# Kernel optimization log

Hardware: AMD Instinct MI355X
Metric: run time of the kernel (lower is better)

The kernel has to match this reference:

```python
import jax, jax.numpy as jnp
import numpy as np

N = 100000   # nodes
E = 1600000  # edges
IN = 32      # in_channels
ED = 16      # edge_dim
G = 128      # num graphs in batch
NEG = 0.01   # LeakyReLU default slope

def lrelu(v):
    return jnp.where(v > 0, v, NEG * v)

def gine_conv(x, src, dst, edge_attr, We, be, Wa, ba, Wb, bb):
    # PyG GINEConv (eps=0): out = nn(x + sum_{j->i} relu(x_j + lin(edge_attr)))
    e = edge_attr @ We + be                      # [E, d]
    m = jax.nn.relu(x[src] + e)                  # gather + add + relu
    agg = jax.ops.segment_sum(m, dst, num_segments=x.shape[0])
    h = x + agg
    return lrelu(h @ Wa + ba) @ Wb + bb

def setup_inputs() -> dict:
    key = jax.random.key(0)
    ks = jax.random.split(key, 24)
    w = lambda k, shape: (jax.random.normal(k, shape, dtype=jnp.float32) * 0.05)
    inp = {
        "x": jax.random.normal(ks[0], (N, IN), dtype=jnp.float32),
        "edge_index": jax.random.randint(ks[1], (2, E), 0, N),
        "edge_attr": jax.random.normal(ks[2], (E, ED), dtype=jnp.float32),
        "batch": jnp.sort(jax.random.randint(ks[3], (N,), 0, G)),
        # conv1: edge lin ED->IN, nn IN->32->64
        "We1": w(ks[4], (ED, IN)), "be1": w(ks[5], (IN,)),
        "W1a": w(ks[6], (IN, 32)), "b1a": w(ks[7], (32,)),
        "W1b": w(ks[8], (32, 64)), "b1b": w(ks[9], (64,)),
        # conv2: edge lin ED->64, nn 64->128->256
        "We2": w(ks[10], (ED, 64)), "be2": w(ks[11], (64,)),
        "W2a": w(ks[12], (64, 128)), "b2a": w(ks[13], (128,)),
        "W2b": w(ks[14], (128, 256)), "b2b": w(ks[15], (256,)),
        # head
        "Wf0": w(ks[16], (256, 128)), "bf0": w(ks[17], (128,)),
        "Wf1": w(ks[18], (128, 64)), "bf1": w(ks[19], (64,)),
        "Wf2": w(ks[20], (64, 32)), "bf2": w(ks[21], (32,)),
        "Wr": w(ks[22], (32, 1)), "br": w(ks[23], (1,)),
    }
    return inp

def reference(x, edge_index, edge_attr, batch,
              We1, be1, W1a, b1a, W1b, b1b,
              We2, be2, W2a, b2a, W2b, b2b,
              Wf0, bf0, Wf1, bf1, Wf2, bf2, Wr, br):
    src, dst = edge_index[0], edge_index[1]
    h = gine_conv(x, src, dst, edge_attr, We1, be1, W1a, b1a, W1b, b1b)
    h = lrelu(h)
    h = gine_conv(h, src, dst, edge_attr, We2, be2, W2a, b2a, W2b, b2b)
    h = lrelu(h)
    # global_add_pool over graph ids
    g = jax.ops.segment_sum(h, batch, num_segments=G)   # [G, 256]
    g = lrelu(g @ Wf0 + bf0)
    # dropout: identity (inference reference)
    g = lrelu(g @ Wf1 + bf1)
    g = lrelu(g @ Wf2 + bf2)
    out = (g @ Wr + br)[:, 0]                           # squeeze(dim=1)
    return out
```

## Files before the change

kernel.cpp:

```cpp
#include <hip/hip_runtime.h>

__device__ __forceinline__ float lrelu(float v){ return v > 0.f ? v : 0.01f*v; }

typedef __attribute__((ext_vector_type(8))) short v8s;
typedef __attribute__((ext_vector_type(4))) float v4f;

__device__ __forceinline__ unsigned short f2bf(float f){
    union{float f; unsigned int i;} v; v.f = f;
    unsigned int u = v.i;
    return (unsigned short)((u + 0x7fffu + ((u >> 16) & 1u)) >> 16);
}
__device__ __forceinline__ unsigned int pack2(float a, float b){
    return (unsigned int)f2bf(a) | ((unsigned int)f2bf(b) << 16);
}
__device__ __forceinline__ float bflo(unsigned int u){
    union{unsigned int i; float f;} v; v.i = u << 16; return v.f;
}
__device__ __forceinline__ float bfhi(unsigned int u){
    union{unsigned int i; float f;} v; v.i = u & 0xffff0000u; return v.f;
}
__device__ __forceinline__ float bf2f(unsigned short s){
    union{unsigned int i; float f;} v; v.i = ((unsigned int)s) << 16; return v.f;
}

__global__ __launch_bounds__(256) void k_hist(
    const int* __restrict__ ei, int* __restrict__ deg, int E)
{
    int e = blockIdx.x * 256 + threadIdx.x;
    if (e >= E) return;
    atomicAdd(&deg[ei[E + e]], 1);
}

__global__ __launch_bounds__(256) void k_scan1(
    const int* __restrict__ deg, int* __restrict__ rowptr,
    int* __restrict__ bsum, int N)
{
    __shared__ int sh[256];
    int t = threadIdx.x;
    int i = blockIdx.x * 256 + t;
    int v = (i < N) ? deg[i] : 0;
    sh[t] = v;
    __syncthreads();
    #pragma unroll
    for (int off = 1; off < 256; off <<= 1) {
        int add = (t >= off) ? sh[t - off] : 0;
        __syncthreads();
        sh[t] += add;
        __syncthreads();
    }
    if (i < N) rowptr[i] = sh[t] - v;
    if (t == 255) bsum[blockIdx.x] = sh[t];
}

__global__ __launch_bounds__(512) void k_scan2(int* __restrict__ bsum, int nb)
{
    __shared__ int sh[512];
    int t = threadIdx.x;
    int v = (t < nb) ? bsum[t] : 0;
    sh[t] = v;
    __syncthreads();
    #pragma unroll
    for (int off = 1; off < 512; off <<= 1) {
        int add = (t >= off) ? sh[t - off] : 0;
        __syncthreads();
        sh[t] += add;
        __syncthreads();
    }
    if (t < nb) bsum[t] = sh[t] - v;
}

__global__ __launch_bounds__(256) void k_scan3(
    int* __restrict__ rowptr, int* __restrict__ cursor,
    const int* __restrict__ bsum, int N)
{
    int i = blockIdx.x * 256 + threadIdx.x;
    if (i >= N) return;
    int rp = rowptr[i] + bsum[i >> 8];
    rowptr[i] = rp;
    cursor[i] = rp;
}

__global__ __launch_bounds__(256) void k_castx(
    const float* __restrict__ x, unsigned int* __restrict__ xb, int M8)
{
    int i = blockIdx.x * 256 + threadIdx.x;
    if (i >= M8) return;
    const float4* p = reinterpret_cast<const float4*>(x) + (size_t)i * 2;
    float4 a = p[0], b = p[1];
    uint4 o;
    o.x = pack2(a.x, a.y); o.y = pack2(a.z, a.w);
    o.z = pack2(b.x, b.y); o.w = pack2(b.z, b.w);
    reinterpret_cast<uint4*>(xb)[i] = o;
}

__global__ __launch_bounds__(256) void k_castw(
    const float* __restrict__ W2a, const float* __restrict__ W2b,
    const float* __restrict__ We1, const float* __restrict__ We2,
    unsigned short* __restrict__ W2aT, unsigned short* __restrict__ W2bT,
    unsigned short* __restrict__ WeT1, unsigned short* __restrict__ WeT2)
{
    int i = blockIdx.x * 256 + threadIdx.x;
    if (i < 128 * 64) {
        int n = i >> 6, k = i & 63;
        W2aT[i] = f2bf(W2a[k * 128 + n]);
    }
    int j = i - 128 * 64;
    if (j >= 0 && j < 256 * 128) {
        int n = j >> 7, k = j & 127;
        W2bT[j] = f2bf(W2b[k * 256 + n]);
    }
    int q1 = i - (128 * 64 + 256 * 128);
    if (q1 >= 0 && q1 < 32 * 32) {
        int cch = q1 >> 5, k = q1 & 31;
        WeT1[q1] = (k < 16) ? f2bf(We1[k * 32 + cch]) : (unsigned short)0;
    }
    int q2 = q1 - 32 * 32;
    if (q2 >= 0 && q2 < 64 * 32) {
        int cch = q2 >> 5, k = q2 & 31;
        WeT2[q2] = (k < 16) ? f2bf(We2[k * 64 + cch]) : (unsigned short)0;
    }
}

__global__ __launch_bounds__(256) void k_scatter(
    const int* __restrict__ ei, const float* __restrict__ ea,
    int* __restrict__ cursor, int2* __restrict__ csr2,
    uint4* __restrict__ eab, int E)
{
    int e = blockIdx.x * 256 + threadIdx.x;
    if (e >= E) return;
    int s = ei[e];
    int d = ei[E + e];
    int slot = atomicAdd(&cursor[d], 1);
    const float4* p = reinterpret_cast<const float4*>(ea) + (size_t)e * 4;
    float4 a = p[0], b = p[1], c = p[2], f = p[3];
    uint4 o0, o1;
    o0.x = pack2(a.x, a.y); o0.y = pack2(a.z, a.w);
    o0.z = pack2(b.x, b.y); o0.w = pack2(b.z, b.w);
    o1.x = pack2(c.x, c.y); o1.y = pack2(c.z, c.w);
    o1.z = pack2(f.x, f.y); o1.w = pack2(f.z, f.w);
    eab[(size_t)slot * 2]     = o0;
    eab[(size_t)slot * 2 + 1] = o1;
    int2 r; r.x = s; r.y = d;
    csr2[slot] = r;
}

#define AGG_SPW 64

__global__ __launch_bounds__(256) void k_agg2(
    const unsigned short* __restrict__ xb,
    const uint4* __restrict__ eab,
    const unsigned short* __restrict__ WeT,
    const float* __restrict__ be,
    const int2* __restrict__ csr2, float* __restrict__ agg, int E)
{
    __shared__ __align__(16) float lds[4][2][16][68];
    const int tid  = threadIdx.x;
    const int wv   = tid >> 6;
    const int lane = tid & 63;
    const int lid  = lane & 15;
    const int quad = lane >> 4;
    const int wave = __builtin_amdgcn_readfirstlane((blockIdx.x * 256 + tid) >> 6);
    const int s0 = wave * AGG_SPW;
    if (s0 >= E) return;
    const int nsl = (s0 + AGG_SPW <= E) ? AGG_SPW : E - s0;

    v8s af0 = *reinterpret_cast<const v8s*>(WeT + lid * 32 + quad * 8);
    v8s af1 = *reinterpret_cast<const v8s*>(WeT + (16 + lid) * 32 + quad * 8);
    v8s af2 = *reinterpret_cast<const v8s*>(WeT + (32 + lid) * 32 + quad * 8);
    v8s af3 = *reinterpret_cast<const v8s*>(WeT + (48 + lid) * 32 + quad * 8);
    const float biasc = be[lane];
    const int2*  cp = csr2 + s0;
    const uint4* ep = eab + (size_t)s0 * 2;

    unsigned short xv[2][16];
    int dsv[2][16];
    float acc = 0.f;
    int   cur = cp[0].y;
    bool  owned = false;

    auto GATHER = [&](int t) {
        const int base = t * 16;
        const int cnt = nsl - base;
        #pragma unroll
        for (int e = 0; e < 16; ++e) {
            int ee = (e < cnt) ? e : cnt - 1;
            int2 r = cp[base + ee];
            dsv[t & 1][e] = r.y;
            xv[t & 1][e] = xb[(unsigned)r.x * 64u + (unsigned)lane];
        }
    };
    auto MFMA = [&](int t) {
        int sl = t * 16 + lid;
        if (sl > nsl - 1) sl = nsl - 1;
        uint4 bw = {0u, 0u, 0u, 0u};
        if (quad < 2) bw = ep[2 * sl + quad];
        union { uint4 u; v8s s; } uu; uu.u = bw;
        v8s bf = uu.s;
        v4f d0 = {0.f, 0.f, 0.f, 0.f}, d1 = d0, d2 = d0, d3 = d0;
        d0 = __builtin_amdgcn_mfma_f32_16x16x32_bf16(af0, bf, d0, 0, 0, 0);
        d1 = __builtin_amdgcn_mfma_f32_16x16x32_bf16(af1, bf, d1, 0, 0, 0);
        d2 = __builtin_amdgcn_mfma_f32_16x16x32_bf16(af2, bf, d2, 0, 0, 0);
        d3 = __builtin_amdgcn_mfma_f32_16x16x32_bf16(af3, bf, d3, 0, 0, 0);
        float* lp = &lds[wv][t & 1][lid][quad * 4];
        *reinterpret_cast<v4f*>(lp)      = d0;
        *reinterpret_cast<v4f*>(lp + 16) = d1;
        *reinterpret_cast<v4f*>(lp + 32) = d2;
        *reinterpret_cast<v4f*>(lp + 48) = d3;
    };
    auto ACCUM = [&](int t) {
        const int cnt = nsl - t * 16;
        #pragma unroll
        for (int e = 0; e < 16; ++e) {
            if (e < cnt) {
                float ls = lds[wv][t & 1][e][lane];
                float m = ls + biasc + bf2f(xv[t & 1][e]);
                m = m > 0.f ? m : 0.f;
                int d = dsv[t & 1][e];
                if (d != cur) {
                    if (owned) agg[(unsigned)cur * 64u + lane] = acc;
                    else       atomicAdd(&agg[(unsigned)cur * 64u + lane], acc);
                    acc = 0.f; cur = d; owned = true;
                }
                acc += m;
            }
        }
    };

    GATHER(0); MFMA(0);
    #pragma unroll
    for (int t = 0; t < 4; ++t) {
        if (t * 16 < nsl) {
            if ((t + 1) < 4 && (t + 1) * 16 < nsl) { GATHER(t + 1); MFMA(t + 1); }
            ACCUM(t);
        }
    }
    atomicAdd(&agg[(unsigned)cur * 64u + lane], acc);
}

__global__ __launch_bounds__(256) void k_agg1(
    const unsigned short* __restrict__ xb,
    const uint4* __restrict__ eab,
    const unsigned short* __restrict__ WeT,
    const float* __restrict__ be,
    const int2* __restrict__ csr2, float* __restrict__ agg, int E)
{
    __shared__ __align__(16) float lds[4][2][16][36];
    const int tid  = threadIdx.x;
    const int wv   = tid >> 6;
    const int lane = tid & 63;
    const int lid  = lane & 15;
    const int quad = lane >> 4;
    const int c    = lane & 31;
    const int sub  = lane >> 5;
    const int wave = __builtin_amdgcn_readfirstlane((blockIdx.x * 256 + tid) >> 6);
    const int s0 = wave * AGG_SPW;
    if (s0 >= E) return;
    const int nsl = (s0 + AGG_SPW <= E) ? AGG_SPW : E - s0;

    v8s af0 = *reinterpret_cast<const v8s*>(WeT + lid * 32 + quad * 8);
    v8s af1 = *reinterpret_cast<const v8s*>(WeT + (16 + lid) * 32 + quad * 8);
    const float biasc = be[c];
    const int2*  cp = csr2 + s0;
    const uint4* ep = eab + (size_t)s0 * 2;

    unsigned short xv[2][8];
    int dsv[2][8];
    float acc = 0.f;
    int cur = cp[(sub < nsl) ? sub : 0].y;

    auto GATHER = [&](int t) {
        #pragma unroll
        for (int i = 0; i < 8; ++i) {
            int e = t * 16 + 2 * i + sub;
            int ee = (e < nsl) ? e : nsl - 1;
            int2 r = cp[ee];
            dsv[t & 1][i] = r.y;
            xv[t & 1][i] = xb[(unsigned)r.x * 32u + (unsigned)c];
        }
    };
    auto MFMA = [&](int t) {
        int sl = t * 16 + lid;
        if (sl > nsl - 1) sl = nsl - 1;
        uint4 bw = {0u, 0u, 0u, 0u};
        if (quad < 2) bw = ep[2 * sl + quad];
        union { uint4 u; v8s s; } uu; uu.u = bw;
        v8s bf = uu.s;
        v4f d0 = {0.f, 0.f, 0.f, 0.f}, d1 = d0;
        d0 = __builtin_amdgcn_mfma_f32_16x16x32_bf16(af0, bf, d0, 0, 0, 0);
        d1 = __builtin_amdgcn_mfma_f32_16x16x32_bf16(af1, bf, d1, 0, 0, 0);
        float* lp = &lds[wv][t & 1][lid][quad * 4];
        *reinterpret_cast<v4f*>(lp)      = d0;
        *reinterpret_cast<v4f*>(lp + 16) = d1;
    };
    auto ACCUM = [&](int t) {
        #pragma unroll
        for (int i = 0; i < 8; ++i) {
            int e = t * 16 + 2 * i + sub;
            if (e < nsl) {
                float ls = lds[wv][t & 1][2 * i + sub][c];
                float m = ls + biasc + bf2f(xv[t & 1][i]);
                m = m > 0.f ? m : 0.f;
                int d = dsv[t & 1][i];
                if (d != cur) {
                    atomicAdd(&agg[(unsigned)cur * 32u + c], acc);
                    acc = 0.f; cur = d;
                }
                acc += m;
            }
        }
    };

    GATHER(0); MFMA(0);
    #pragma unroll
    for (int t = 0; t < 4; ++t) {
        if (t * 16 < nsl) {
            if ((t + 1) < 4 && (t + 1) * 16 < nsl) { GATHER(t + 1); MFMA(t + 1); }
            ACCUM(t);
        }
    }
    atomicAdd(&agg[(unsigned)cur * 32u + c], acc);
}

__global__ __launch_bounds__(256, 4) void k_mlp1(
    const float* __restrict__ x, const float* __restrict__ agg1,
    const float* __restrict__ W1a, const float* __restrict__ b1a,
    const float* __restrict__ W1b, const float* __restrict__ b1b,
    float* __restrict__ h1, unsigned int* __restrict__ h1b, int N)
{
    __shared__ float ts[64][33];
    const int tid = threadIdx.x;
    const int n0 = blockIdx.x * 64;
    const int row = tid & 63;
    const int grp = __builtin_amdgcn_readfirstlane(tid >> 6);
    const int g = n0 + row;

    float hv[32];
    if (g < N) {
        const float4* xp = reinterpret_cast<const float4*>(x) + (size_t)g * 8;
        const float4* ap = reinterpret_cast<const float4*>(agg1) + (size_t)g * 8;
        #pragma unroll
        for (int q = 0; q < 8; ++q) {
            float4 a = xp[q], b = ap[q];
            hv[4*q+0]=a.x+b.x; hv[4*q+1]=a.y+b.y;
            hv[4*q+2]=a.z+b.z; hv[4*q+3]=a.w+b.w;
        }
    } else {
        #pragma unroll
        for (int q = 0; q < 32; ++q) hv[q] = 0.f;
    }

    {
        const int c0 = grp * 8;
        float acc[8];
        #pragma unroll
        for (int i = 0; i < 8; ++i) acc[i] = b1a[c0 + i];
        for (int k = 0; k < 32; ++k) {
            float h = hv[k];
            const float* w = W1a + k*32 + c0;
            #pragma unroll
            for (int i = 0; i < 8; ++i) acc[i] = fmaf(h, w[i], acc[i]);
        }
        #pragma unroll
        for (int i = 0; i < 8; ++i) ts[row][c0 + i] = lrelu(acc[i]);
    }
    __syncthreads();

    {
        const int c0 = grp * 16;
        float acc[16];
        #pragma unroll
        for (int i = 0; i < 16; ++i) acc[i] = b1b[c0 + i];
        for (int k = 0; k < 32; ++k) {
            float tv = ts[row][k];
            const float* w = W1b + k*64 + c0;
            #pragma unroll
            for (int i = 0; i < 16; ++i) acc[i] = fmaf(tv, w[i], acc[i]);
        }
        if (g < N) {
            #pragma unroll
            for (int i = 0; i < 16; ++i) acc[i] = lrelu(acc[i]);
            float4* op = reinterpret_cast<float4*>(h1) + (size_t)g*16 + (c0>>2);
            #pragma unroll
            for (int q = 0; q < 4; ++q) {
                float4 o;
                o.x = acc[4*q+0]; o.y = acc[4*q+1];
                o.z = acc[4*q+2]; o.w = acc[4*q+3];
                op[q] = o;
            }
            uint4 p0, p1;
            p0.x = pack2(acc[0],  acc[1]);  p0.y = pack2(acc[2],  acc[3]);
            p0.z = pack2(acc[4],  acc[5]);  p0.w = pack2(acc[6],  acc[7]);
            p1.x = pack2(acc[8],  acc[9]);  p1.y = pack2(acc[10], acc[11]);
            p1.z = pack2(acc[12], acc[13]); p1.w = pack2(acc[14], acc[15]);
            uint4* bp = reinterpret_cast<uint4*>(h1b + (size_t)g*32 + (c0>>1));
            bp[0] = p0; bp[1] = p1;
        }
    }
}

__global__ __launch_bounds__(256) void k_mlp2(
    const float* __restrict__ h1, const float* __restrict__ agg2,
    const unsigned short* __restrict__ W2aT, const float* __restrict__ b2a,
    const unsigned short* __restrict__ W2bT, const float* __restrict__ b2b,
    unsigned short* __restrict__ h2b, int N)
{
    __shared__ unsigned short hs[64][72];
    __shared__ unsigned short ts[64][136];
    const int tid = threadIdx.x;
    const int n0 = blockIdx.x * 64;

    {
        int r = tid >> 2, cseg = (tid & 3) * 16;
        int g = n0 + r;
        uint4 o0 = {0,0,0,0}, o1 = {0,0,0,0};
        if (g < N) {
            const float4* xp = reinterpret_cast<const float4*>(h1)
                               + (size_t)g*16 + (cseg>>2);
            const float4* ap = reinterpret_cast<const float4*>(agg2)
                               + (size_t)g*16 + (cseg>>2);
            float4 a0=xp[0], a1=xp[1], a2=xp[2], a3=xp[3];
            float4 b0=ap[0], b1=ap[1], b2=ap[2], b3=ap[3];
            o0.x = pack2(a0.x+b0.x, a0.y+b0.y); o0.y = pack2(a0.z+b0.z, a0.w+b0.w);
            o0.z = pack2(a1.x+b1.x, a1.y+b1.y); o0.w = pack2(a1.z+b1.z, a1.w+b1.w);
            o1.x = pack2(a2.x+b2.x, a2.y+b2.y); o1.y = pack2(a2.z+b2.z, a2.w+b2.w);
            o1.z = pack2(a3.x+b3.x, a3.y+b3.y); o1.w = pack2(a3.z+b3.z, a3.w+b3.w);
        }
        uint4* dp = reinterpret_cast<uint4*>(&hs[r][cseg]);
        dp[0] = o0; dp[1] = o1;
    }
    __syncthreads();

    const int wv   = __builtin_amdgcn_readfirstlane(tid >> 6);
    const int lane = tid & 63;
    const int lid  = lane & 15;
    const int quad = lane >> 4;

    v8s afA0 = *reinterpret_cast<const v8s*>(&hs[wv*16 + lid][quad*8]);
    v8s afA1 = *reinterpret_cast<const v8s*>(&hs[wv*16 + lid][32 + quad*8]);
    #pragma unroll
    for (int nt = 0; nt < 8; ++nt) {
        v4f acc = {0.f, 0.f, 0.f, 0.f};
        const unsigned short* wp = W2aT + (nt*16 + lid)*64 + quad*8;
        v8s b0 = *reinterpret_cast<const v8s*>(wp);
        v8s b1 = *reinterpret_cast<const v8s*>(wp + 32);
        acc = __builtin_amdgcn_mfma_f32_16x16x32_bf16(afA0, b0, acc, 0, 0, 0);
        acc = __builtin_amdgcn_mfma_f32_16x16x32_bf16(afA1, b1, acc, 0, 0, 0);
        float bias = b2a[nt*16 + lid];
        #pragma unroll
        for (int i = 0; i < 4; ++i) {
            float v = lrelu(acc[i] + bias);
            ts[wv*16 + quad*4 + i][nt*16 + lid] = f2bf(v);
        }
    }
    __syncthreads();

    v8s afB[4];
    #pragma unroll
    for (int ks = 0; ks < 4; ++ks)
        afB[ks] = *reinterpret_cast<const v8s*>(&ts[wv*16 + lid][ks*32 + quad*8]);
    const int gbase = n0 + wv*16 + quad*4;
    #pragma unroll 4
    for (int nt = 0; nt < 16; ++nt) {
        v4f acc = {0.f, 0.f, 0.f, 0.f};
        const unsigned short* wp = W2bT + (nt*16 + lid)*128 + quad*8;
        #pragma unroll
        for (int ks = 0; ks < 4; ++ks) {
            v8s bf = *reinterpret_cast<const v8s*>(wp + ks*32);
            acc = __builtin_amdgcn_mfma_f32_16x16x32_bf16(afB[ks], bf, acc, 0, 0, 0);
        }
        float bias = b2b[nt*16 + lid];
        #pragma unroll
        for (int i = 0; i < 4; ++i) {
            int g = gbase + i;
            if (g < N) {
                float v = lrelu(acc[i] + bias);
                h2b[(size_t)g*256 + nt*16 + lid] = f2bf(v);
            }
        }
    }
}

__global__ __launch_bounds__(256) void k_pool(
    const unsigned int* __restrict__ h2b, const int* __restrict__ batch,
    float* __restrict__ g, int N)
{
    int tid = threadIdx.x;
    int c2 = tid & 127;
    int h = tid >> 7;
    int base = blockIdx.x * 128;
    int n0 = base + h;
    int nend = base + 128; if (nend > N) nend = N;
    if (n0 >= N) return;
    float acc0 = 0.f, acc1 = 0.f;
    int cur = batch[n0];
    for (int n = n0; n < nend; n += 2) {
        int b = batch[n];
        unsigned int hv = h2b[(size_t)n * 128 + c2];
        if (b != cur) {
            atomicAdd(&g[(unsigned)cur * 256 + 2*c2],     acc0);
            atomicAdd(&g[(unsigned)cur * 256 + 2*c2 + 1], acc1);
            acc0 = acc1 = 0.f; cur = b;
        }
        acc0 += bflo(hv); acc1 += bfhi(hv);
    }
    atomicAdd(&g[(unsigned)cur * 256 + 2*c2],     acc0);
    atomicAdd(&g[(unsigned)cur * 256 + 2*c2 + 1], acc1);
}

__global__ __launch_bounds__(256) void k_head(
    const float* __restrict__ g,
    const float* __restrict__ Wf0, const float* __restrict__ bf0,
    const float* __restrict__ Wf1, const float* __restrict__ bf1,
    const float* __restrict__ Wf2, const float* __restrict__ bf2,
    const float* __restrict__ Wr,  const float* __restrict__ br,
    float* __restrict__ out)
{
    __shared__ float buf[256];
    __shared__ float t0[128];
    __shared__ float t1[64];
    __shared__ float t2[32];
    int gid = blockIdx.x, tid = threadIdx.x;
    buf[tid] = g[(size_t)gid*256 + tid];
    __syncthreads();
    if (tid < 128) {
        float acc = bf0[tid];
        for (int k = 0; k < 256; ++k) acc = fmaf(buf[k], Wf0[k*128 + tid], acc);
        t0[tid] = lrelu(acc);
    }
    __syncthreads();
    if (tid < 64) {
        float acc = bf1[tid];
        for (int k = 0; k < 128; ++k) acc = fmaf(t0[k], Wf1[k*64 + tid], acc);
        t1[tid] = lrelu(acc);
    }
    __syncthreads();
    if (tid < 32) {
        float acc = bf2[tid];
        for (int k = 0; k < 64; ++k) acc = fmaf(t1[k], Wf2[k*32 + tid], acc);
        t2[tid] = lrelu(acc);
    }
    __syncthreads();
    if (tid == 0) {
        float acc = br[0];
        for (int k = 0; k < 32; ++k) acc = fmaf(t2[k], Wr[k], acc);
        out[gid] = acc;
    }
}

extern "C" void kernel_launch(void* const* d_in, const int* in_sizes, int n_in,
                              void* d_out, int out_size, void* d_ws, size_t ws_size,
                              hipStream_t stream)
{
    const float* x     = (const float*)d_in[0];
    const int*   ei    = (const int*)d_in[1];
    const float* ea    = (const float*)d_in[2];
    const int*   batch = (const int*)d_in[3];
    const float* We1=(const float*)d_in[4],  *be1=(const float*)d_in[5];
    const float* W1a=(const float*)d_in[6],  *b1a=(const float*)d_in[7];
    const float* W1b=(const float*)d_in[8],  *b1b=(const float*)d_in[9];
    const float* We2=(const float*)d_in[10], *be2=(const float*)d_in[11];
    const float* W2a=(const float*)d_in[12], *b2a=(const float*)d_in[13];
    const float* W2b=(const float*)d_in[14], *b2b=(const float*)d_in[15];
    const float* Wf0=(const float*)d_in[16], *bf0=(const float*)d_in[17];
    const float* Wf1=(const float*)d_in[18], *bf1=(const float*)d_in[19];
    const float* Wf2=(const float*)d_in[20], *bf2=(const float*)d_in[21];
    const float* Wr =(const float*)d_in[22], *br =(const float*)d_in[23];

    const int N = in_sizes[0] / 32;
    const int E = in_sizes[1] / 2;
    const int G = out_size;
    const int nb = (N + 255) / 256;
    const int nb64 = (N + 63) / 64;

    char* p = (char*)d_ws;
    int*   deg     = (int*)p;                 p += (size_t)N * 4;
    float* gbuf    = (float*)p;               p += (size_t)G * 256 * 4;
    float* agg1    = (float*)p;               p += (size_t)N * 32 * 4;
    float* agg2    = (float*)p;               p += (size_t)N * 64 * 4;
    size_t zero_bytes = (size_t)(p - (char*)d_ws);
    int*   rowptr  = (int*)p;                 p += (size_t)N * 4;
    int*   cursor  = (int*)p;                 p += (size_t)N * 4;
    int*   bsum    = (int*)p;                 p += 512 * 4;
    p = (char*)(((uintptr_t)p + 15) & ~(uintptr_t)15);
    int2*  csr2    = (int2*)p;                p += (size_t)E * 8;
    uint4* eab     = (uint4*)p;               p += (size_t)E * 32;
    unsigned short* xb   = (unsigned short*)p; p += (size_t)N * 32 * 2;
    float* h1      = (float*)p;               p += (size_t)N * 64 * 4;
    unsigned int*   h1b  = (unsigned int*)p;  p += (size_t)N * 64 * 2;
    unsigned short* W2aT = (unsigned short*)p; p += 128 * 64 * 2;
    unsigned short* W2bT = (unsigned short*)p; p += 256 * 128 * 2;
    unsigned short* WeT1 = (unsigned short*)p; p += 32 * 32 * 2;
    unsigned short* WeT2 = (unsigned short*)p; p += 64 * 32 * 2;
    unsigned short* h2b  = (unsigned short*)p; p += (size_t)N * 256 * 2;

    hipMemsetAsync(d_ws, 0, zero_bytes, stream);

    int eb = (E + 255) / 256;

    k_hist   <<<eb, 256, 0, stream>>>(ei, deg, E);
    k_scan1  <<<nb, 256, 0, stream>>>(deg, rowptr, bsum, N);
    k_scan2  <<<1, 512, 0, stream>>>(bsum, nb);
    k_scan3  <<<nb, 256, 0, stream>>>(rowptr, cursor, bsum, N);
    {
        int M8 = N * 32 / 8;
        k_castx<<<(M8 + 255) / 256, 256, 0, stream>>>(x, (unsigned int*)xb, M8);
    }
    {
        int tot = 128*64 + 256*128 + 32*32 + 64*32;
        k_castw<<<(tot + 255) / 256, 256, 0, stream>>>(W2a, W2b, We1, We2,
                                                       W2aT, W2bT, WeT1, WeT2);
    }
    k_scatter<<<eb, 256, 0, stream>>>(ei, ea, cursor, csr2, eab, E);

    {
        int waves = (E + AGG_SPW - 1) / AGG_SPW;
        int blocks = (waves + 3) / 4;
        k_agg1<<<blocks, 256, 0, stream>>>(xb, eab, WeT1, be1, csr2, agg1, E);
    }
    k_mlp1<<<nb64, 256, 0, stream>>>(x, agg1, W1a, b1a, W1b, b1b, h1,
                                     (unsigned int*)h1b, N);

    {
        int waves = (E + AGG_SPW - 1) / AGG_SPW;
        int blocks = (waves + 3) / 4;
        k_agg2<<<blocks, 256, 0, stream>>>((const unsigned short*)h1b, eab, WeT2,
                                           be2, csr2, agg2, E);
    }
    k_mlp2<<<nb64, 256, 0, stream>>>(h1, agg2, W2aT, b2a, W2bT, b2b, h2b, N);

    k_pool<<<(N + 127) / 128, 256, 0, stream>>>((const unsigned int*)h2b, batch,
                                                gbuf, N);
    k_head<<<G, 256, 0, stream>>>(gbuf, Wf0, bf0, Wf1, bf1, Wf2, bf2, Wr, br,
                                  (float*)d_out);
}
```

Baseline: 626.3 us.

## Interleave edge index and features into 64B records; drop fp32 h1 buffer

Combines the per-slot (src,dst) pair and bf16 edge attributes into one cache-line-aligned 64-byte record so the aggregation kernels touch a single stream per edge. It also removes the fp32 copy of the first-layer output, and the second MLP reads the bf16 copy for its residual. The padding raises total edge-record bytes written and read. Reading h1 in bf16 slightly reduces the precision of the residual sum.

```diff
diff --git a/kernel.cpp b/kernel.cpp
--- a/kernel.cpp
+++ b/kernel.cpp
@@ -123,8 +123,7 @@
 
 __global__ __launch_bounds__(256) void k_scatter(
     const int* __restrict__ ei, const float* __restrict__ ea,
-    int* __restrict__ cursor, int2* __restrict__ csr2,
-    uint4* __restrict__ eab, int E)
+    int* __restrict__ cursor, uint4* __restrict__ recs, int E)
 {
     int e = blockIdx.x * 256 + threadIdx.x;
     if (e >= E) return;
@@ -133,25 +132,25 @@
     int slot = atomicAdd(&cursor[d], 1);
     const float4* p = reinterpret_cast<const float4*>(ea) + (size_t)e * 4;
     float4 a = p[0], b = p[1], c = p[2], f = p[3];
-    uint4 o0, o1;
+    uint4 o0, o1, o2, o3;
     o0.x = pack2(a.x, a.y); o0.y = pack2(a.z, a.w);
     o0.z = pack2(b.x, b.y); o0.w = pack2(b.z, b.w);
     o1.x = pack2(c.x, c.y); o1.y = pack2(c.z, c.w);
     o1.z = pack2(f.x, f.y); o1.w = pack2(f.z, f.w);
-    eab[(size_t)slot * 2]     = o0;
-    eab[(size_t)slot * 2 + 1] = o1;
-    int2 r; r.x = s; r.y = d;
-    csr2[slot] = r;
+    o2.x = (unsigned)s; o2.y = (unsigned)d; o2.z = 0u; o2.w = 0u;
+    o3.x = 0u; o3.y = 0u; o3.z = 0u; o3.w = 0u;
+    uint4* rp = recs + (size_t)slot * 4;
+    rp[0] = o0; rp[1] = o1; rp[2] = o2; rp[3] = o3;
 }
 
 #define AGG_SPW 64
 
 __global__ __launch_bounds__(256) void k_agg2(
     const unsigned short* __restrict__ xb,
-    const uint4* __restrict__ eab,
+    const uint4* __restrict__ recs,
     const unsigned short* __restrict__ WeT,
     const float* __restrict__ be,
-    const int2* __restrict__ csr2, float* __restrict__ agg, int E)
+    float* __restrict__ agg, int E)
 {
     __shared__ __align__(16) float lds[4][2][16][68];
     const int tid  = threadIdx.x;
@@ -169,13 +168,12 @@
     v8s af2 = *reinterpret_cast<const v8s*>(WeT + (32 + lid) * 32 + quad * 8);
     v8s af3 = *reinterpret_cast<const v8s*>(WeT + (48 + lid) * 32 + quad * 8);
     const float biasc = be[lane];
-    const int2*  cp = csr2 + s0;
-    const uint4* ep = eab + (size_t)s0 * 2;
+    const uint4* rp = recs + (size_t)s0 * 4;
 
     unsigned short xv[2][16];
     int dsv[2][16];
     float acc = 0.f;
-    int   cur = cp[0].y;
+    int   cur = reinterpret_cast<const int2*>(rp + 2)->y;
     bool  owned = false;
 
     auto GATHER = [&](int t) {
@@ -184,7 +182,7 @@
         #pragma unroll
         for (int e = 0; e < 16; ++e) {
             int ee = (e < cnt) ? e : cnt - 1;
-            int2 r = cp[base + ee];
+            int2 r = *reinterpret_cast<const int2*>(rp + (base + ee) * 4 + 2);
             dsv[t & 1][e] = r.y;
             xv[t & 1][e] = xb[(unsigned)r.x * 64u + (unsigned)lane];
         }
@@ -193,7 +191,7 @@
         int sl = t * 16 + lid;
         if (sl > nsl - 1) sl = nsl - 1;
         uint4 bw = {0u, 0u, 0u, 0u};
-        if (quad < 2) bw = ep[2 * sl + quad];
+        if (quad < 2) bw = rp[sl * 4 + quad];
         union { uint4 u; v8s s; } uu; uu.u = bw;
         v8s bf = uu.s;
         v4f d0 = {0.f, 0.f, 0.f, 0.f}, d1 = d0, d2 = d0, d3 = d0;
@@ -239,10 +237,10 @@
 
 __global__ __launch_bounds__(256) void k_agg1(
     const unsigned short* __restrict__ xb,
-    const uint4* __restrict__ eab,
+    const uint4* __restrict__ recs,
     const unsigned short* __restrict__ WeT,
     const float* __restrict__ be,
-    const int2* __restrict__ csr2, float* __restrict__ agg, int E)
+    float* __restrict__ agg, int E)
 {
     __shared__ __align__(16) float lds[4][2][16][36];
     const int tid  = threadIdx.x;
@@ -260,20 +258,19 @@
     v8s af0 = *reinterpret_cast<const v8s*>(WeT + lid * 32 + quad * 8);
     v8s af1 = *reinterpret_cast<const v8s*>(WeT + (16 + lid) * 32 + quad * 8);
     const float biasc = be[c];
-    const int2*  cp = csr2 + s0;
-    const uint4* ep = eab + (size_t)s0 * 2;
+    const uint4* rp = recs + (size_t)s0 * 4;
 
     unsigned short xv[2][8];
     int dsv[2][8];
     float acc = 0.f;
-    int cur = cp[(sub < nsl) ? sub : 0].y;
+    int cur = reinterpret_cast<const int2*>(rp + ((sub < nsl) ? sub : 0) * 4 + 2)->y;
 
     auto GATHER = [&](int t) {
         #pragma unroll
         for (int i = 0; i < 8; ++i) {
             int e = t * 16 + 2 * i + sub;
             int ee = (e < nsl) ? e : nsl - 1;
-            int2 r = cp[ee];
+            int2 r = *reinterpret_cast<const int2*>(rp + ee * 4 + 2);
             dsv[t & 1][i] = r.y;
             xv[t & 1][i] = xb[(unsigned)r.x * 32u + (unsigned)c];
         }
@@ -282,7 +279,7 @@
         int sl = t * 16 + lid;
         if (sl > nsl - 1) sl = nsl - 1;
         uint4 bw = {0u, 0u, 0u, 0u};
-        if (quad < 2) bw = ep[2 * sl + quad];
+        if (quad < 2) bw = rp[sl * 4 + quad];
         union { uint4 u; v8s s; } uu; uu.u = bw;
         v8s bf = uu.s;
         v4f d0 = {0.f, 0.f, 0.f, 0.f}, d1 = d0;
@@ -325,7 +322,7 @@
     const float* __restrict__ x, const float* __restrict__ agg1,
     const float* __restrict__ W1a, const float* __restrict__ b1a,
     const float* __restrict__ W1b, const float* __restrict__ b1b,
-    float* __restrict__ h1, unsigned int* __restrict__ h1b, int N)
+    unsigned int* __restrict__ h1b, int N)
 {
     __shared__ float ts[64][33];
     const int tid = threadIdx.x;
@@ -379,14 +376,6 @@
         if (g < N) {
             #pragma unroll
             for (int i = 0; i < 16; ++i) acc[i] = lrelu(acc[i]);
-            float4* op = reinterpret_cast<float4*>(h1) + (size_t)g*16 + (c0>>2);
-            #pragma unroll
-            for (int q = 0; q < 4; ++q) {
-                float4 o;
-                o.x = acc[4*q+0]; o.y = acc[4*q+1];
-                o.z = acc[4*q+2]; o.w = acc[4*q+3];
-                op[q] = o;
-            }
             uint4 p0, p1;
             p0.x = pack2(acc[0],  acc[1]);  p0.y = pack2(acc[2],  acc[3]);
             p0.z = pack2(acc[4],  acc[5]);  p0.w = pack2(acc[6],  acc[7]);
@@ -399,7 +388,7 @@
 }
 
 __global__ __launch_bounds__(256) void k_mlp2(
-    const float* __restrict__ h1, const float* __restrict__ agg2,
+    const unsigned int* __restrict__ h1b, const float* __restrict__ agg2,
     const unsigned short* __restrict__ W2aT, const float* __restrict__ b2a,
     const unsigned short* __restrict__ W2bT, const float* __restrict__ b2b,
     unsigned short* __restrict__ h2b, int N)
@@ -414,16 +403,20 @@
         int g = n0 + r;
         uint4 o0 = {0,0,0,0}, o1 = {0,0,0,0};
         if (g < N) {
-            const float4* xp = reinterpret_cast<const float4*>(h1)
-                               + (size_t)g*16 + (cseg>>2);
+            const uint4* hp = reinterpret_cast<const uint4*>(
+                                  h1b + (size_t)g*32 + (cseg>>1));
             const float4* ap = reinterpret_cast<const float4*>(agg2)
                                + (size_t)g*16 + (cseg>>2);
-            float4 a0=xp[0], a1=xp[1], a2=xp[2], a3=xp[3];
+            uint4 u0 = hp[0], u1 = hp[1];
             float4 b0=ap[0], b1=ap[1], b2=ap[2], b3=ap[3];
-            o0.x = pack2(a0.x+b0.x, a0.y+b0.y); o0.y = pack2(a0.z+b0.z, a0.w+b0.w);
-            o0.z = pack2(a1.x+b1.x, a1.y+b1.y); o0.w = pack2(a1.z+b1.z, a1.w+b1.w);
-            o1.x = pack2(a2.x+b2.x, a2.y+b2.y); o1.y = pack2(a2.z+b2.z, a2.w+b2.w);
-            o1.z = pack2(a3.x+b3.x, a3.y+b3.y); o1.w = pack2(a3.z+b3.z, a3.w+b3.w);
+            o0.x = pack2(bflo(u0.x)+b0.x, bfhi(u0.x)+b0.y);
+            o0.y = pack2(bflo(u0.y)+b0.z, bfhi(u0.y)+b0.w);
+            o0.z = pack2(bflo(u0.z)+b1.x, bfhi(u0.z)+b1.y);
+            o0.w = pack2(bflo(u0.w)+b1.z, bfhi(u0.w)+b1.w);
+            o1.x = pack2(bflo(u1.x)+b2.x, bfhi(u1.x)+b2.y);
+            o1.y = pack2(bflo(u1.y)+b2.z, bfhi(u1.y)+b2.w);
+            o1.z = pack2(bflo(u1.z)+b3.x, bfhi(u1.z)+b3.y);
+            o1.w = pack2(bflo(u1.w)+b3.z, bfhi(u1.w)+b3.w);
         }
         uint4* dp = reinterpret_cast<uint4*>(&hs[r][cseg]);
         dp[0] = o0; dp[1] = o1;
@@ -581,11 +574,9 @@
     int*   rowptr  = (int*)p;                 p += (size_t)N * 4;
     int*   cursor  = (int*)p;                 p += (size_t)N * 4;
     int*   bsum    = (int*)p;                 p += 512 * 4;
-    p = (char*)(((uintptr_t)p + 15) & ~(uintptr_t)15);
-    int2*  csr2    = (int2*)p;                p += (size_t)E * 8;
-    uint4* eab     = (uint4*)p;               p += (size_t)E * 32;
+    p = (char*)(((uintptr_t)p + 63) & ~(uintptr_t)63);
+    uint4* recs    = (uint4*)p;               p += (size_t)E * 64;
     unsigned short* xb   = (unsigned short*)p; p += (size_t)N * 32 * 2;
-    float* h1      = (float*)p;               p += (size_t)N * 64 * 4;
     unsigned int*   h1b  = (unsigned int*)p;  p += (size_t)N * 64 * 2;
     unsigned short* W2aT = (unsigned short*)p; p += 128 * 64 * 2;
     unsigned short* W2bT = (unsigned short*)p; p += 256 * 128 * 2;
@@ -610,23 +601,23 @@
         k_castw<<<(tot + 255) / 256, 256, 0, stream>>>(W2a, W2b, We1, We2,
                                                        W2aT, W2bT, WeT1, WeT2);
     }
-    k_scatter<<<eb, 256, 0, stream>>>(ei, ea, cursor, csr2, eab, E);
+    k_scatter<<<eb, 256, 0, stream>>>(ei, ea, cursor, recs, E);
 
     {
         int waves = (E + AGG_SPW - 1) / AGG_SPW;
         int blocks = (waves + 3) / 4;
-        k_agg1<<<blocks, 256, 0, stream>>>(xb, eab, WeT1, be1, csr2, agg1, E);
-    }
-    k_mlp1<<<nb64, 256, 0, stream>>>(x, agg1, W1a, b1a, W1b, b1b, h1,
+        k_agg1<<<blocks, 256, 0, stream>>>(xb, recs, WeT1, be1, agg1, E);
+    }
+    k_mlp1<<<nb64, 256, 0, stream>>>(x, agg1, W1a, b1a, W1b, b1b,
                                      (unsigned int*)h1b, N);
 
     {
         int waves = (E + AGG_SPW - 1) / AGG_SPW;
         int blocks = (waves + 3) / 4;
-        k_agg2<<<blocks, 256, 0, stream>>>((const unsigned short*)h1b, eab, WeT2,
-                                           be2, csr2, agg2, E);
-    }
-    k_mlp2<<<nb64, 256, 0, stream>>>(h1, agg2, W2aT, b2a, W2bT, b2b, h2b, N);
+        k_agg2<<<blocks, 256, 0, stream>>>((const unsigned short*)h1b, recs, WeT2,
+                                           be2, agg2, E);
+    }
+    k_mlp2<<<nb64, 256, 0, stream>>>(h1b, agg2, W2aT, b2a, W2bT, b2b, h2b, N);
 
     k_pool<<<(N + 127) / 128, 256, 0, stream>>>((const unsigned int*)h2b, batch,
                                                 gbuf, N);
```

After: 666.1 us. 6.3% more time.

## Partition edge scatter by destination range and drop fp32 h1 buffer

Applied to the files above, without the earlier changes.

The scatter kernel now has each edge chunk processed by 8 blocks. Each block keeps only the edges whose destination falls in one eighth of the node range, so the scattered writes and cursor atomics from a block land in a narrower address window and stay more cache-local. The cost is that the destination index array is read 8 times. Separately, the fp32 h1 output is removed: mlp2 now reads the bf16 h1b copy, which halves that read and removes a large write. The residual add in mlp2 therefore uses bf16-rounded h1 values, and the workspace alignment is raised to 64 bytes.

```diff
diff --git a/kernel.cpp b/kernel.cpp
--- a/kernel.cpp
+++ b/kernel.cpp
@@ -121,27 +121,37 @@
     }
 }
 
+#define RCHUNK 2048
 __global__ __launch_bounds__(256) void k_scatter(
     const int* __restrict__ ei, const float* __restrict__ ea,
     int* __restrict__ cursor, int2* __restrict__ csr2,
-    uint4* __restrict__ eab, int E)
-{
-    int e = blockIdx.x * 256 + threadIdx.x;
-    if (e >= E) return;
-    int s = ei[e];
-    int d = ei[E + e];
-    int slot = atomicAdd(&cursor[d], 1);
-    const float4* p = reinterpret_cast<const float4*>(ea) + (size_t)e * 4;
-    float4 a = p[0], b = p[1], c = p[2], f = p[3];
-    uint4 o0, o1;
-    o0.x = pack2(a.x, a.y); o0.y = pack2(a.z, a.w);
-    o0.z = pack2(b.x, b.y); o0.w = pack2(b.z, b.w);
-    o1.x = pack2(c.x, c.y); o1.y = pack2(c.z, c.w);
-    o1.z = pack2(f.x, f.y); o1.w = pack2(f.z, f.w);
-    eab[(size_t)slot * 2]     = o0;
-    eab[(size_t)slot * 2 + 1] = o1;
-    int2 r; r.x = s; r.y = d;
-    csr2[slot] = r;
+    uint4* __restrict__ eab, int E, int N)
+{
+    const int r = blockIdx.x & 7;
+    const int c = blockIdx.x >> 3;
+    const int rspan = (N + 7) >> 3;
+    const int lo = r * rspan;
+    const int hi = lo + rspan;
+    int base = c * RCHUNK;
+    int end = base + RCHUNK; if (end > E) end = E;
+    for (int e = base + threadIdx.x; e < end; e += 256) {
+        int d = ei[E + e];
+        if (d >= lo && d < hi) {
+            int s = ei[e];
+            int slot = atomicAdd(&cursor[d], 1);
+            const float4* p = reinterpret_cast<const float4*>(ea) + (size_t)e * 4;
+            float4 a = p[0], b = p[1], cc = p[2], f = p[3];
+            uint4 o0, o1;
+            o0.x = pack2(a.x, a.y);  o0.y = pack2(a.z, a.w);
+            o0.z = pack2(b.x, b.y);  o0.w = pack2(b.z, b.w);
+            o1.x = pack2(cc.x, cc.y); o1.y = pack2(cc.z, cc.w);
+            o1.z = pack2(f.x, f.y);  o1.w = pack2(f.z, f.w);
+            eab[(size_t)slot * 2]     = o0;
+            eab[(size_t)slot * 2 + 1] = o1;
+            int2 rr; rr.x = s; rr.y = d;
+            csr2[slot] = rr;
+        }
+    }
 }
 
 #define AGG_SPW 64
@@ -325,7 +335,7 @@
     const float* __restrict__ x, const float* __restrict__ agg1,
     const float* __restrict__ W1a, const float* __restrict__ b1a,
     const float* __restrict__ W1b, const float* __restrict__ b1b,
-    float* __restrict__ h1, unsigned int* __restrict__ h1b, int N)
+    unsigned int* __restrict__ h1b, int N)
 {
     __shared__ float ts[64][33];
     const int tid = threadIdx.x;
@@ -379,14 +389,6 @@
         if (g < N) {
             #pragma unroll
             for (int i = 0; i < 16; ++i) acc[i] = lrelu(acc[i]);
-            float4* op = reinterpret_cast<float4*>(h1) + (size_t)g*16 + (c0>>2);
-            #pragma unroll
-            for (int q = 0; q < 4; ++q) {
-                float4 o;
-                o.x = acc[4*q+0]; o.y = acc[4*q+1];
-                o.z = acc[4*q+2]; o.w = acc[4*q+3];
-                op[q] = o;
-            }
             uint4 p0, p1;
             p0.x = pack2(acc[0],  acc[1]);  p0.y = pack2(acc[2],  acc[3]);
             p0.z = pack2(acc[4],  acc[5]);  p0.w = pack2(acc[6],  acc[7]);
@@ -399,7 +401,7 @@
 }
 
 __global__ __launch_bounds__(256) void k_mlp2(
-    const float* __restrict__ h1, const float* __restrict__ agg2,
+    const unsigned int* __restrict__ h1b, const float* __restrict__ agg2,
     const unsigned short* __restrict__ W2aT, const float* __restrict__ b2a,
     const unsigned short* __restrict__ W2bT, const float* __restrict__ b2b,
     unsigned short* __restrict__ h2b, int N)
@@ -414,16 +416,20 @@
         int g = n0 + r;
         uint4 o0 = {0,0,0,0}, o1 = {0,0,0,0};
         if (g < N) {
-            const float4* xp = reinterpret_cast<const float4*>(h1)
-                               + (size_t)g*16 + (cseg>>2);
+            const uint4* hp = reinterpret_cast<const uint4*>(
+                                  h1b + (size_t)g*32 + (cseg>>1));
             const float4* ap = reinterpret_cast<const float4*>(agg2)
                                + (size_t)g*16 + (cseg>>2);
-            float4 a0=xp[0], a1=xp[1], a2=xp[2], a3=xp[3];
+            uint4 u0 = hp[0], u1 = hp[1];
             float4 b0=ap[0], b1=ap[1], b2=ap[2], b3=ap[3];
-            o0.x = pack2(a0.x+b0.x, a0.y+b0.y); o0.y = pack2(a0.z+b0.z, a0.w+b0.w);
-            o0.z = pack2(a1.x+b1.x, a1.y+b1.y); o0.w = pack2(a1.z+b1.z, a1.w+b1.w);
-            o1.x = pack2(a2.x+b2.x, a2.y+b2.y); o1.y = pack2(a2.z+b2.z, a2.w+b2.w);
-            o1.z = pack2(a3.x+b3.x, a3.y+b3.y); o1.w = pack2(a3.z+b3.z, a3.w+b3.w);
+            o0.x = pack2(bflo(u0.x)+b0.x, bfhi(u0.x)+b0.y);
+            o0.y = pack2(bflo(u0.y)+b0.z, bfhi(u0.y)+b0.w);
+            o0.z = pack2(bflo(u0.z)+b1.x, bfhi(u0.z)+b1.y);
+            o0.w = pack2(bflo(u0.w)+b1.z, bfhi(u0.w)+b1.w);
+            o1.x = pack2(bflo(u1.x)+b2.x, bfhi(u1.x)+b2.y);
+            o1.y = pack2(bflo(u1.y)+b2.z, bfhi(u1.y)+b2.w);
+            o1.z = pack2(bflo(u1.z)+b3.x, bfhi(u1.z)+b3.y);
+            o1.w = pack2(bflo(u1.w)+b3.z, bfhi(u1.w)+b3.w);
         }
         uint4* dp = reinterpret_cast<uint4*>(&hs[r][cseg]);
         dp[0] = o0; dp[1] = o1;
@@ -581,11 +587,10 @@
     int*   rowptr  = (int*)p;                 p += (size_t)N * 4;
     int*   cursor  = (int*)p;                 p += (size_t)N * 4;
     int*   bsum    = (int*)p;                 p += 512 * 4;
-    p = (char*)(((uintptr_t)p + 15) & ~(uintptr_t)15);
+    p = (char*)(((uintptr_t)p + 63) & ~(uintptr_t)63);
     int2*  csr2    = (int2*)p;                p += (size_t)E * 8;
     uint4* eab     = (uint4*)p;               p += (size_t)E * 32;
     unsigned short* xb   = (unsigned short*)p; p += (size_t)N * 32 * 2;
-    float* h1      = (float*)p;               p += (size_t)N * 64 * 4;
     unsigned int*   h1b  = (unsigned int*)p;  p += (size_t)N * 64 * 2;
     unsigned short* W2aT = (unsigned short*)p; p += 128 * 64 * 2;
     unsigned short* W2bT = (unsigned short*)p; p += 256 * 128 * 2;
@@ -610,14 +615,18 @@
         k_castw<<<(tot + 255) / 256, 256, 0, stream>>>(W2a, W2b, We1, We2,
                                                        W2aT, W2bT, WeT1, WeT2);
     }
-    k_scatter<<<eb, 256, 0, stream>>>(ei, ea, cursor, csr2, eab, E);
+    {
+        int nchunks = (E + RCHUNK - 1) / RCHUNK;
+        k_scatter<<<nchunks * 8, 256, 0, stream>>>(ei, ea, cursor, csr2, eab,
+                                                   E, N);
+    }
 
     {
         int waves = (E + AGG_SPW - 1) / AGG_SPW;
         int blocks = (waves + 3) / 4;
         k_agg1<<<blocks, 256, 0, stream>>>(xb, eab, WeT1, be1, csr2, agg1, E);
     }
-    k_mlp1<<<nb64, 256, 0, stream>>>(x, agg1, W1a, b1a, W1b, b1b, h1,
+    k_mlp1<<<nb64, 256, 0, stream>>>(x, agg1, W1a, b1a, W1b, b1b,
                                      (unsigned int*)h1b, N);
 
     {
@@ -626,7 +635,7 @@
         k_agg2<<<blocks, 256, 0, stream>>>((const unsigned short*)h1b, eab, WeT2,
                                            be2, csr2, agg2, E);
     }
-    k_mlp2<<<nb64, 256, 0, stream>>>(h1, agg2, W2aT, b2a, W2bT, b2b, h2b, N);
+    k_mlp2<<<nb64, 256, 0, stream>>>(h1b, agg2, W2aT, b2a, W2bT, b2b, h2b, N);
 
     k_pool<<<(N + 127) / 128, 256, 0, stream>>>((const unsigned int*)h2b, batch,
                                                 gbuf, N);
```

New measurement: 678.7 us. 1.08x slower.
